# Kernel tuning notes

Hardware: AMD Instinct MI355X
Metric: run time of the kernel (lower is better)

Reference implementation:

```python
import jax, jax.numpy as jnp
import numpy as np

EMB_SIZE = 768
NUM_HEADS = 8


def setup_inputs() -> dict:
    key = jax.random.key(0)
    ks = jax.random.split(key, 6)
    B, N, E = 8, 1024, EMB_SIZE
    return {
        "x": jax.random.normal(ks[0], (B, N, E), dtype=jnp.float32),
        "relative_pos": jax.random.normal(ks[1], (NUM_HEADS, N, N), dtype=jnp.float32),
        "qkv_w": jax.random.normal(ks[2], (2 * E, E), dtype=jnp.float32) * 0.02,
        "qkv_b": jax.random.normal(ks[3], (2 * E,), dtype=jnp.float32) * 0.02,
        "val_w": jax.random.normal(ks[4], (E, E), dtype=jnp.float32) * 0.02,
        "val_b": jax.random.normal(ks[5], (E,), dtype=jnp.float32) * 0.02,
    }


def reference(x, relative_pos, qkv_w, qkv_b, val_w, val_b):
    B, N, E = x.shape
    H = NUM_HEADS
    D = E // H
    # qkv projection: [B, N, 2E]; last dim layout is (h, d, qk) per einops rearrange
    qkv = (x @ qkv_w.T + qkv_b).reshape(B, N, H, D, 2)
    q = jnp.transpose(qkv[..., 0], (0, 2, 1, 3))  # [B, H, N, D]
    k = jnp.transpose(qkv[..., 1], (0, 2, 1, 3))  # [B, H, N, D]
    scale = E ** 0.5  # original divides by sqrt(emb_size), not sqrt(d_head)
    energy = jnp.einsum('bhqd,bhkd->bhqk', q, k) / scale  # [B, H, N, N]
    # relative_pos [H, N, N] broadcasts over batch
    energy = jax.nn.softmax(energy + relative_pos, axis=-1)
    values = x @ val_w.T + val_b  # [B, N, E]
    return values, energy
```

## Files before the change

kernel.cpp:

```cpp
#include <hip/hip_runtime.h>
#include <hip/hip_bf16.h>

#define EMB 768
#define NH 8
#define DH 96
#define BATCH 8
#define SEQ 1024
#define M_TOT (BATCH * SEQ)
#define NCOLS (3 * EMB)

typedef float f32x4 __attribute__((ext_vector_type(4)));
typedef __bf16 bf16x8 __attribute__((ext_vector_type(8)));

__device__ __forceinline__ unsigned short f2bf_bits(float f) {
  __hip_bfloat16 b = __float2bfloat16(f);
  return *reinterpret_cast<unsigned short*>(&b);
}

__device__ __forceinline__ void gload_lds16(const void* g, void* l) {
  __builtin_amdgcn_global_load_lds(
      (__attribute__((address_space(1))) void*)(g),
      (__attribute__((address_space(3))) void*)(l), 16, 0, 0);
}

__global__ void prep_x_kernel(const float* __restrict__ x, __hip_bfloat16* __restrict__ xb) {
  const int n4 = M_TOT * EMB / 4;
  int i = blockIdx.x * blockDim.x + threadIdx.x;
  if (i < n4) {
    f32x4 v = reinterpret_cast<const f32x4*>(x)[i];
    ushort4 o;
    o.x = f2bf_bits(v[0]);
    o.y = f2bf_bits(v[1]);
    o.z = f2bf_bits(v[2]);
    o.w = f2bf_bits(v[3]);
    reinterpret_cast<ushort4*>(xb)[i] = o;
  }
}

__global__ void prep_w_kernel(const float* __restrict__ qkv_w, const float* __restrict__ qkv_b,
                              const float* __restrict__ val_w, const float* __restrict__ val_b,
                              __hip_bfloat16* __restrict__ Wall, float* __restrict__ bias) {
  const float inv_s = 0.03608439182435161f;
  int idx = blockIdx.x * 256 + threadIdx.x;
  if (idx >= NCOLS * EMB) return;
  int r = idx / EMB;
  int c = idx - r * EMB;
  float v;
  if (r < EMB) {
    int h = r / DH, d = r - h * DH;
    int src = h * 192 + 2 * d;
    v = qkv_w[(size_t)src * EMB + c] * inv_s;
    if (c == 0) bias[r] = qkv_b[src] * inv_s;
  } else if (r < 2 * EMB) {
    int r2 = r - EMB;
    int h = r2 / DH, d = r2 - h * DH;
    int src = h * 192 + 2 * d + 1;
    v = qkv_w[(size_t)src * EMB + c];
    if (c == 0) bias[r] = qkv_b[src];
  } else {
    int r3 = r - 2 * EMB;
    v = val_w[(size_t)r3 * EMB + c];
    if (c == 0) bias[r] = val_b[r3];
  }
  Wall[idx] = __float2bfloat16(v);
}

__global__ __launch_bounds__(256) void gemm_kernel(
    const __hip_bfloat16* __restrict__ xb, const __hip_bfloat16* __restrict__ Wall,
    const float* __restrict__ bias, __hip_bfloat16* __restrict__ qhead,
    __hip_bfloat16* __restrict__ khead, float* __restrict__ vout) {
  __shared__ __hip_bfloat16 As[128 * 32];
  __shared__ __hip_bfloat16 Bs[128 * 32];
  __shared__ __hip_bfloat16 Cs[128][136];
  const int tid = threadIdx.x;
  const int w = tid >> 6, l = tid & 63;
  const int m0 = blockIdx.x * 128;
  const int n0 = blockIdx.y * 128;
  const int wr = w >> 1, wc = w & 1;

  f32x4 acc[4][4] = {};

  const int sr0 = (w * 2 + 0) * 16 + (l >> 2);
  const int sr1 = (w * 2 + 1) * 16 + (l >> 2);
  const int sc = (l & 3) * 8;

  for (int kt = 0; kt < EMB / 32; ++kt) {
    const int k0 = kt * 32;
    gload_lds16(xb + (size_t)(m0 + sr0) * EMB + k0 + sc, (void*)(As + (w * 2 + 0) * 512));
    gload_lds16(xb + (size_t)(m0 + sr1) * EMB + k0 + sc, (void*)(As + (w * 2 + 1) * 512));
    gload_lds16(Wall + (size_t)(n0 + sr0) * EMB + k0 + sc, (void*)(Bs + (w * 2 + 0) * 512));
    gload_lds16(Wall + (size_t)(n0 + sr1) * EMB + k0 + sc, (void*)(Bs + (w * 2 + 1) * 512));
    __syncthreads();

    bf16x8 af[4], bfr[4];
#pragma unroll
    for (int t = 0; t < 4; ++t) {
      af[t] = *reinterpret_cast<const bf16x8*>(As + (wr * 64 + t * 16 + (l & 15)) * 32 + (l >> 4) * 8);
      bfr[t] = *reinterpret_cast<const bf16x8*>(Bs + (wc * 64 + t * 16 + (l & 15)) * 32 + (l >> 4) * 8);
    }
#pragma unroll
    for (int i = 0; i < 4; ++i)
#pragma unroll
      for (int j = 0; j < 4; ++j)
        acc[i][j] = __builtin_amdgcn_mfma_f32_16x16x32_bf16(af[i], bfr[j], acc[i][j], 0, 0, 0);
    __syncthreads();
  }

  if (n0 >= 2 * EMB) {
    const int rowbase = m0 + wr * 64;
    const int colbase = n0 - 2 * EMB + wc * 64;
#pragma unroll
    for (int j = 0; j < 4; ++j) {
      const int n = colbase + j * 16 + (l & 15);
      const float bb = bias[2 * EMB + n];
#pragma unroll
      for (int i = 0; i < 4; ++i) {
#pragma unroll
        for (int q = 0; q < 4; ++q) {
          const int m = rowbase + i * 16 + (l >> 4) * 4 + q;
          vout[(size_t)m * EMB + n] = acc[i][j][q] + bb;
        }
      }
    }
  } else {
#pragma unroll
    for (int j = 0; j < 4; ++j) {
      const int nl = wc * 64 + j * 16 + (l & 15);
      const float bb = bias[n0 + nl];
#pragma unroll
      for (int i = 0; i < 4; ++i) {
#pragma unroll
        for (int q = 0; q < 4; ++q) {
          const int ml = wr * 64 + i * 16 + (l >> 4) * 4 + q;
          Cs[ml][nl] = __float2bfloat16(acc[i][j][q] + bb);
        }
      }
    }
    __syncthreads();
    __hip_bfloat16* dst = (n0 >= EMB) ? khead : qhead;
    const int ch0 = (n0 >= EMB) ? (n0 - EMB) : n0;
    const int cg = (tid & 15) * 8;
    const int gch = ch0 + cg;
    const int hh = gch / DH, dd = gch - hh * DH;
#pragma unroll
    for (int pass = 0; pass < 8; ++pass) {
      const int r = pass * 16 + (tid >> 4);
      const int m = m0 + r;
      const int bb_ = m >> 10, mm = m & 1023;
      bf16x8 v8 = *reinterpret_cast<const bf16x8*>(&Cs[r][cg]);
      *reinterpret_cast<bf16x8*>(dst + ((size_t)(bb_ * NH + hh) * SEQ + mm) * DH + dd) = v8;
    }
  }
}

__global__ __launch_bounds__(512, 2) void attn_kernel(
    const __hip_bfloat16* __restrict__ qhead, const __hip_bfloat16* __restrict__ khead,
    const float* __restrict__ rel, float* __restrict__ eout) {
  __shared__ alignas(16) char KS[8 * 3 * 3072];
  __shared__ float redm[16][8];
  __shared__ float reds[16][8];

  const int t = threadIdx.x;
  const int w = t >> 6, l = t & 63;
  const int lr = l >> 4, lc = l & 15;
  const int flat = blockIdx.x;
  const int u = flat >> 6;
  const int b = (flat >> 3) & 7;
  const int g = u * 8 + (flat & 7);
  const int h = g >> 6;
  const int rb = g & 63;
  const int row0 = rb * 16;
  const size_t bh = (size_t)(b * NH + h);

  const __hip_bfloat16* qsrc = qhead + (bh * SEQ + row0 + lc) * DH;
  bf16x8 qf[3];
#pragma unroll
  for (int kc = 0; kc < 3; ++kc)
    qf[kc] = *reinterpret_cast<const bf16x8*>(qsrc + kc * 32 + lr * 8);

  const float* relsrc = rel + ((size_t)h * SEQ + row0 + lc) * SEQ + w * 128 + lr * 4;
  f32x4 relv[8];
#pragma unroll
  for (int s = 0; s < 8; ++s)
    relv[s] = *reinterpret_cast<const f32x4*>(relsrc + s * 16);

  const __hip_bfloat16* ksrc = khead + bh * SEQ * DH + (size_t)w * 128 * DH;
  char* kdst = KS + w * 9216;

#define STAGE_K(s, buf)                                                             \
  {                                                                                 \
    const __hip_bfloat16* s_ = ksrc + (size_t)(s) * 1536 + (size_t)l * 8;           \
    gload_lds16(s_, kdst + (buf) * 3072);                                           \
    gload_lds16(s_ + 512, kdst + (buf) * 3072 + 1024);                              \
    gload_lds16(s_ + 1024, kdst + (buf) * 3072 + 2048);                             \
  }

  STAGE_K(0, 0)
  STAGE_K(1, 1)

  f32x4 acc[8];
#pragma unroll
  for (int s = 0; s < 8; ++s) {
    if (s < 6) STAGE_K(s + 2, (s + 2) % 3)
    if (s < 6) {
      asm volatile("s_waitcnt vmcnt(6)" ::: "memory");
    } else if (s == 6) {
      asm volatile("s_waitcnt vmcnt(3)" ::: "memory");
    } else {
      asm volatile("s_waitcnt vmcnt(0)" ::: "memory");
    }
    __builtin_amdgcn_sched_barrier(0);
    const __hip_bfloat16* kp =
        reinterpret_cast<const __hip_bfloat16*>(kdst + (s % 3) * 3072) + lc * DH;
    f32x4 a = {0.f, 0.f, 0.f, 0.f};
    __builtin_amdgcn_s_setprio(1);
#pragma unroll
    for (int kc = 0; kc < 3; ++kc) {
      bf16x8 kf = *reinterpret_cast<const bf16x8*>(kp + kc * 32 + lr * 8);
      a = __builtin_amdgcn_mfma_f32_16x16x32_bf16(kf, qf[kc], a, 0, 0, 0);
    }
    __builtin_amdgcn_s_setprio(0);
    acc[s] = a + relv[s];
  }
#undef STAGE_K

  float mx = -3.4e38f;
#pragma unroll
  for (int s = 0; s < 8; ++s)
    mx = fmaxf(mx, fmaxf(fmaxf(acc[s][0], acc[s][1]), fmaxf(acc[s][2], acc[s][3])));
  mx = fmaxf(mx, __shfl_xor(mx, 16));
  mx = fmaxf(mx, __shfl_xor(mx, 32));
  if (l < 16) redm[lc][w] = mx;
  __syncthreads();
  float M = redm[lc][0];
#pragma unroll
  for (int i = 1; i < 8; ++i) M = fmaxf(M, redm[lc][i]);

  float sm = 0.f;
#pragma unroll
  for (int s = 0; s < 8; ++s) {
#pragma unroll
    for (int j = 0; j < 4; ++j) {
      float e = __expf(acc[s][j] - M);
      acc[s][j] = e;
      sm += e;
    }
  }
  sm += __shfl_xor(sm, 16);
  sm += __shfl_xor(sm, 32);
  if (l < 16) reds[lc][w] = sm;
  __syncthreads();
  float S = 0.f;
#pragma unroll
  for (int i = 0; i < 8; ++i) S += reds[lc][i];
  const float rinv = 1.0f / S;

  float* op = eout + (bh * SEQ + row0 + lc) * SEQ + w * 128 + lr * 4;
#pragma unroll
  for (int s = 0; s < 8; ++s) {
    f32x4 v = acc[s] * rinv;
    __builtin_nontemporal_store(v, reinterpret_cast<f32x4*>(op + s * 16));
  }
}

extern "C" void kernel_launch(void* const* d_in, const int* in_sizes, int n_in,
                              void* d_out, int out_size, void* d_ws, size_t ws_size,
                              hipStream_t stream) {
  const float* x = (const float*)d_in[0];
  const float* rel = (const float*)d_in[1];
  const float* qkv_w = (const float*)d_in[2];
  const float* qkv_b = (const float*)d_in[3];
  const float* val_w = (const float*)d_in[4];
  const float* val_b = (const float*)d_in[5];
  float* out = (float*)d_out;

  char* ws = (char*)d_ws;
  __hip_bfloat16* xb = (__hip_bfloat16*)(ws);
  __hip_bfloat16* Wall = (__hip_bfloat16*)(ws + 12582912);
  float* bias = (float*)(ws + 16121856);
  __hip_bfloat16* qhead = (__hip_bfloat16*)(ws + 16131072);
  __hip_bfloat16* khead = (__hip_bfloat16*)(ws + 28713984);

  float* vout = out;
  float* eout = out + (size_t)M_TOT * EMB;

  prep_x_kernel<<<dim3(M_TOT * EMB / 4 / 256), dim3(256), 0, stream>>>(x, xb);
  prep_w_kernel<<<dim3(NCOLS * EMB / 256), dim3(256), 0, stream>>>(qkv_w, qkv_b, val_w, val_b,
                                                                   Wall, bias);
  gemm_kernel<<<dim3(M_TOT / 128, NCOLS / 128), dim3(256), 0, stream>>>(xb, Wall, bias, qhead,
                                                                        khead, vout);
  attn_kernel<<<dim3(SEQ / 16 * NH * BATCH), dim3(512), 0, stream>>>(qhead, khead, rel, eout);
}
```

Measured before the change: 161.1 us.

## Merge prep kernels, remap GEMM tile order, use nontemporal value stores

Fuses the x-conversion and weight-prep kernels into one launch that splits work by block index, removing one kernel launch. The GEMM grid becomes 1D with a remapped tile order that spreads consecutive blocks across row tiles, likely for better cache locality or XCD distribution. The fp32 value output is written with nontemporal stores to avoid polluting cache. The remap assumes 64 row tiles and 18 column tiles, so it is hardcoded to these sizes.

```diff
diff --git a/kernel.cpp b/kernel.cpp
--- a/kernel.cpp
+++ b/kernel.cpp
@@ -23,10 +23,15 @@
       (__attribute__((address_space(3))) void*)(l), 16, 0, 0);
 }
 
-__global__ void prep_x_kernel(const float* __restrict__ x, __hip_bfloat16* __restrict__ xb) {
-  const int n4 = M_TOT * EMB / 4;
-  int i = blockIdx.x * blockDim.x + threadIdx.x;
-  if (i < n4) {
+#define PREPX_BLOCKS (M_TOT * EMB / 4 / 256)
+#define PREPW_BLOCKS (NCOLS * EMB / 256)
+__global__ void prep_kernel(const float* __restrict__ x, __hip_bfloat16* __restrict__ xb,
+                            const float* __restrict__ qkv_w, const float* __restrict__ qkv_b,
+                            const float* __restrict__ val_w, const float* __restrict__ val_b,
+                            __hip_bfloat16* __restrict__ Wall, float* __restrict__ bias) {
+  const int bid = blockIdx.x;
+  if (bid < PREPX_BLOCKS) {
+    int i = bid * 256 + threadIdx.x;
     f32x4 v = reinterpret_cast<const f32x4*>(x)[i];
     ushort4 o;
     o.x = f2bf_bits(v[0]);
@@ -34,35 +39,30 @@
     o.z = f2bf_bits(v[2]);
     o.w = f2bf_bits(v[3]);
     reinterpret_cast<ushort4*>(xb)[i] = o;
-  }
-}
-
-__global__ void prep_w_kernel(const float* __restrict__ qkv_w, const float* __restrict__ qkv_b,
-                              const float* __restrict__ val_w, const float* __restrict__ val_b,
-                              __hip_bfloat16* __restrict__ Wall, float* __restrict__ bias) {
-  const float inv_s = 0.03608439182435161f;
-  int idx = blockIdx.x * 256 + threadIdx.x;
-  if (idx >= NCOLS * EMB) return;
-  int r = idx / EMB;
-  int c = idx - r * EMB;
-  float v;
-  if (r < EMB) {
-    int h = r / DH, d = r - h * DH;
-    int src = h * 192 + 2 * d;
-    v = qkv_w[(size_t)src * EMB + c] * inv_s;
-    if (c == 0) bias[r] = qkv_b[src] * inv_s;
-  } else if (r < 2 * EMB) {
-    int r2 = r - EMB;
-    int h = r2 / DH, d = r2 - h * DH;
-    int src = h * 192 + 2 * d + 1;
-    v = qkv_w[(size_t)src * EMB + c];
-    if (c == 0) bias[r] = qkv_b[src];
   } else {
-    int r3 = r - 2 * EMB;
-    v = val_w[(size_t)r3 * EMB + c];
-    if (c == 0) bias[r] = val_b[r3];
-  }
-  Wall[idx] = __float2bfloat16(v);
+    const float inv_s = 0.03608439182435161f;
+    int idx = (bid - PREPX_BLOCKS) * 256 + threadIdx.x;
+    int r = idx / EMB;
+    int c = idx - r * EMB;
+    float v;
+    if (r < EMB) {
+      int h = r / DH, d = r - h * DH;
+      int src = h * 192 + 2 * d;
+      v = qkv_w[(size_t)src * EMB + c] * inv_s;
+      if (c == 0) bias[r] = qkv_b[src] * inv_s;
+    } else if (r < 2 * EMB) {
+      int r2 = r - EMB;
+      int h = r2 / DH, d = r2 - h * DH;
+      int src = h * 192 + 2 * d + 1;
+      v = qkv_w[(size_t)src * EMB + c];
+      if (c == 0) bias[r] = qkv_b[src];
+    } else {
+      int r3 = r - 2 * EMB;
+      v = val_w[(size_t)r3 * EMB + c];
+      if (c == 0) bias[r] = val_b[r3];
+    }
+    Wall[idx] = __float2bfloat16(v);
+  }
 }
 
 __global__ __launch_bounds__(256) void gemm_kernel(
@@ -74,8 +74,13 @@
   __shared__ __hip_bfloat16 Cs[128][136];
   const int tid = threadIdx.x;
   const int w = tid >> 6, l = tid & 63;
-  const int m0 = blockIdx.x * 128;
-  const int n0 = blockIdx.y * 128;
+  const int flat = blockIdx.x;
+  const int a_ = flat & 7;
+  const int tq = flat >> 3;
+  const int b_ = tq % 18;
+  const int c_ = tq / 18;
+  const int m0 = (a_ * 8 + c_) * 128;
+  const int n0 = b_ * 128;
   const int wr = w >> 1, wc = w & 1;
 
   f32x4 acc[4][4] = {};
@@ -118,7 +123,7 @@
 #pragma unroll
         for (int q = 0; q < 4; ++q) {
           const int m = rowbase + i * 16 + (l >> 4) * 4 + q;
-          vout[(size_t)m * EMB + n] = acc[i][j][q] + bb;
+          __builtin_nontemporal_store(acc[i][j][q] + bb, &vout[(size_t)m * EMB + n]);
         }
       }
     }
@@ -284,10 +289,9 @@
   float* vout = out;
   float* eout = out + (size_t)M_TOT * EMB;
 
-  prep_x_kernel<<<dim3(M_TOT * EMB / 4 / 256), dim3(256), 0, stream>>>(x, xb);
-  prep_w_kernel<<<dim3(NCOLS * EMB / 256), dim3(256), 0, stream>>>(qkv_w, qkv_b, val_w, val_b,
-                                                                   Wall, bias);
-  gemm_kernel<<<dim3(M_TOT / 128, NCOLS / 128), dim3(256), 0, stream>>>(xb, Wall, bias, qhead,
-                                                                        khead, vout);
+  prep_kernel<<<dim3(PREPX_BLOCKS + PREPW_BLOCKS), dim3(256), 0, stream>>>(
+      x, xb, qkv_w, qkv_b, val_w, val_b, Wall, bias);
+  gemm_kernel<<<dim3(M_TOT / 128 * (NCOLS / 128)), dim3(256), 0, stream>>>(xb, Wall, bias,
+                                                                           qhead, khead, vout);
   attn_kernel<<<dim3(SEQ / 16 * NH * BATCH), dim3(512), 0, stream>>>(qhead, khead, rel, eout);
 }
```

New measurement: 171.0 us. 1.06x slower.
